# Kernel optimization log

Measured on AMD Instinct MI355X. Metric: run time of the kernel, lower is better.

The kernel has to match this reference:

```python
import jax, jax.numpy as jnp
import numpy as np

N = 8192
IN_DIM, HID_DIM, OUT_DIM = 32, 64, 16


def setup_inputs() -> dict:
    key = jax.random.key(0)
    k1, k2, k3, k4, k5, k6, k7 = jax.random.split(key, 7)
    s1 = 1.0 / np.sqrt(IN_DIM)
    s2 = 1.0 / np.sqrt(HID_DIM)
    return {
        "adj1": jax.random.normal(k1, (N, N), jnp.float32),
        "adj2": jax.random.normal(k2, (N, N), jnp.float32),
        "features": jax.random.normal(k3, (N, IN_DIM), jnp.float32),
        # gc1 linear (shared across both aggregation branches)
        "W1": jax.random.uniform(k4, (IN_DIM, HID_DIM), jnp.float32, -s1, s1),
        "b1": jax.random.uniform(k5, (HID_DIM,), jnp.float32, -s1, s1),
        # gc2 linear
        "W2": jax.random.uniform(k6, (HID_DIM, OUT_DIM), jnp.float32, -s2, s2),
        "b2": jax.random.uniform(k7, (OUT_DIM,), jnp.float32, -s2, s2),
    }


def _gc_layer(adj1, adj2, x, W, b):
    # branch 1: aggregate -> shared linear -> relu
    o1 = jax.nn.relu(jnp.matmul(adj1, x) @ W + b)
    # branch 2: same linear weights
    o2 = jax.nn.relu(jnp.matmul(adj2, x) @ W + b)
    return o1 + o2


def reference(adj1, adj2, features, W1, b1, W2, b2):
    h1 = _gc_layer(adj1, adj2, features, W1, b1)  # [N, HID_DIM]
    h2 = _gc_layer(adj1, adj2, h1, W2, b2)        # [N, OUT_DIM]
    return h2
```

## Files before the change

kernel.cpp:

```cpp
#include <hip/hip_runtime.h>
#include <stdint.h>

#define NN 8192
#define IN_DIM 32
#define HID_DIM 64
#define OUT_DIM 16

typedef __attribute__((ext_vector_type(8))) short short8;
typedef __attribute__((ext_vector_type(4))) float f32x4;

__device__ __forceinline__ short f2bf_bits(float x){
  uint32_t u = __builtin_bit_cast(uint32_t, x);
  u += 0x7FFFu + ((u >> 16) & 1u);
  return (short)(u >> 16);
}

__device__ __forceinline__ short8 cvt8(f32x4 lo, f32x4 hi){
  short8 r;
  r[0]=f2bf_bits(lo[0]); r[1]=f2bf_bits(lo[1]); r[2]=f2bf_bits(lo[2]); r[3]=f2bf_bits(lo[3]);
  r[4]=f2bf_bits(hi[0]); r[5]=f2bf_bits(hi[1]); r[6]=f2bf_bits(hi[2]); r[7]=f2bf_bits(hi[3]);
  return r;
}

__global__ __launch_bounds__(256) void k_g(const float* __restrict__ X, const float* __restrict__ W1,
                                           short* __restrict__ Gt){
  const int b    = blockIdx.x;
  const int rb   = (b & 127) * 64;
  const int cg   = b >> 7;
  const int lane = threadIdx.x & 63;
  const int c    = cg * 4 + (threadIdx.x >> 6);
  const int r    = rb + lane;
  const float* xr = X + (size_t)r * IN_DIM;
  float acc = 0.f;
  #pragma unroll
  for (int k = 0; k < IN_DIM; ++k)
    acc += xr[k] * W1[(size_t)k * HID_DIM + c];
  Gt[(size_t)c * NN + r] = f2bf_bits(acc);
}

template<int REV>
__global__ __launch_bounds__(64, 2) void mm64r(const float* __restrict__ adj1, const float* __restrict__ adj2,
                                               const short* __restrict__ Bt,
                                               float* __restrict__ P1, float* __restrict__ P2, int klen){
  __shared__ __align__(16) float sA[2][64 * 32];
  const int l     = threadIdx.x;
  const int strip = REV ? ((int)gridDim.x - 1 - (int)blockIdx.x) : (int)blockIdx.x;
  const int ks    = REV ? ((int)gridDim.y - 1 - (int)blockIdx.y) : (int)blockIdx.y;
  const int z     = REV ? (1 - (int)blockIdx.z) : (int)blockIdx.z;
  const float* __restrict__ adj = z ? adj2 : adj1;
  const int k0    = ks * klen;
  const int ngrp  = klen >> 5;
  const int phase = (strip + (z << 3)) & (ngrp - 1);
  const int rl    = l & 15;
  const int qh    = l >> 4;
  const int sr8   = l >> 3;
  const int sg    = (l & 7) ^ sr8;
  const size_t rowb = (size_t)strip * 64 * NN;

  auto gmap = [&](int t){
    const int tg = REV ? (phase + ngrp - 1 - t) : (phase + t);
    return tg & (ngrp - 1);
  };

  auto SL = [&](int t, f32x4 (&R)[8]){
    const int g = gmap(t);
    const float* base = adj + rowb + (size_t)(k0 + g * 32) + sg * 4;
    #pragma unroll
    for (int p = 0; p < 8; ++p)
      R[p] = *(const f32x4*)(base + (size_t)(p * 8 + sr8) * NN);
  };

  auto DW = [&](const f32x4 (&R)[8], float* buf){
    float* dst = buf + (l & 7) * 4;
    #pragma unroll
    for (int p = 0; p < 8; ++p)
      *(f32x4*)(dst + (p * 8 + sr8) * 32) = R[p];
  };

  auto BL = [&](int t, short8 (&d)[4]){
    const int g = gmap(t);
    const size_t bk = (size_t)(k0 + g * 32) + qh * 8;
    #pragma unroll
    for (int f = 0; f < 4; ++f)
      d[f] = *(const short8*)(Bt + (size_t)(f * 16 + rl) * NN + bk);
  };

  f32x4 acc[4][4];
  #pragma unroll
  for (int mi = 0; mi < 4; ++mi)
    #pragma unroll
    for (int f = 0; f < 4; ++f)
      acc[mi][f] = f32x4{0.f,0.f,0.f,0.f};

  auto compute = [&](const float* sa, const short8 (&b)[4]){
    #pragma unroll
    for (int mi = 0; mi < 4; ++mi){
      const int row = mi * 16 + rl;
      f32x4 lo = *(const f32x4*)(sa + row * 32 + (((qh * 2    ) ^ (rl & 7)) << 2));
      f32x4 hi = *(const f32x4*)(sa + row * 32 + (((qh * 2 + 1) ^ (rl & 7)) << 2));
      short8 fa = cvt8(lo, hi);
      #pragma unroll
      for (int f = 0; f < 4; ++f)
        acc[mi][f] = __builtin_amdgcn_mfma_f32_16x16x32_bf16(fa, b[f], acc[mi][f], 0, 0, 0);
    }
  };

  f32x4 SA[8];
  short8 bA[4], bB[4];

  SL(0, SA); BL(0, bA);

  #pragma unroll 1
  for (int t = 0; t < ngrp - 2; t += 2){
    asm volatile("s_waitcnt vmcnt(4)" ::: "memory");
    __builtin_amdgcn_sched_barrier(0);
    DW(SA, &sA[0][0]);
    SL(t + 1, SA);
    asm volatile("s_waitcnt vmcnt(8)" ::: "memory");
    __builtin_amdgcn_sched_barrier(0);
    BL(t + 1, bB);
    compute(&sA[0][0], bA);
    asm volatile("s_waitcnt vmcnt(4)" ::: "memory");
    __builtin_amdgcn_sched_barrier(0);
    DW(SA, &sA[1][0]);
    SL(t + 2, SA);
    asm volatile("s_waitcnt vmcnt(8)" ::: "memory");
    __builtin_amdgcn_sched_barrier(0);
    BL(t + 2, bA);
    compute(&sA[1][0], bB);
  }
  asm volatile("s_waitcnt vmcnt(4)" ::: "memory");
  __builtin_amdgcn_sched_barrier(0);
  DW(SA, &sA[0][0]);
  SL(ngrp - 1, SA);
  asm volatile("s_waitcnt vmcnt(8)" ::: "memory");
  __builtin_amdgcn_sched_barrier(0);
  BL(ngrp - 1, bB);
  compute(&sA[0][0], bA);
  asm volatile("s_waitcnt vmcnt(4)" ::: "memory");
  __builtin_amdgcn_sched_barrier(0);
  DW(SA, &sA[1][0]);
  asm volatile("s_waitcnt vmcnt(0)" ::: "memory");
  __builtin_amdgcn_sched_barrier(0);
  compute(&sA[1][0], bB);

  float* P = z ? P2 : P1;
  #pragma unroll
  for (int mi = 0; mi < 4; ++mi){
    const int orow = strip * 64 + mi * 16 + qh * 4;
    float* p = P + ((size_t)ks * NN + orow) * HID_DIM + rl;
    #pragma unroll
    for (int r = 0; r < 4; ++r){
      #pragma unroll
      for (int f = 0; f < 4; ++f)
        p[(size_t)r * HID_DIM + f * 16] = acc[mi][f][r];
    }
  }
}

__global__ __launch_bounds__(256) void l1_combine(const float* __restrict__ Y1p, const float* __restrict__ Y2p,
                                                  const float* __restrict__ b1,
                                                  short* __restrict__ H1t, int S){
  __shared__ float sH[64][65];
  const int tid = threadIdx.x, lane = tid & 63, wave = tid >> 6;
  const int rb = blockIdx.x * 64;
  const float bc = b1[lane];
  #pragma unroll 4
  for (int rq = 0; rq < 16; ++rq){
    const int r = rq * 4 + wave;
    const int row = rb + r;
    float s1 = 0.f, s2 = 0.f;
    for (int sp = 0; sp < S; ++sp){
      s1 += Y1p[((size_t)sp * NN + row) * HID_DIM + lane];
      s2 += Y2p[((size_t)sp * NN + row) * HID_DIM + lane];
    }
    sH[r][lane] = fmaxf(s1 + bc, 0.f) + fmaxf(s2 + bc, 0.f);
  }
  __syncthreads();
  #pragma unroll 4
  for (int i = 0; i < 16; ++i){
    const int c = wave * 16 + i;
    H1t[(size_t)c * NN + rb + lane] = f2bf_bits(sH[lane][c]);
  }
}

__global__ __launch_bounds__(256) void l2_combine(const float* __restrict__ Z1p, const float* __restrict__ Z2p,
                                                  const float* __restrict__ W2, const float* __restrict__ b2,
                                                  float* __restrict__ out, int S){
  __shared__ float sW[HID_DIM * OUT_DIM];
  __shared__ float sb[OUT_DIM];
  __shared__ float sz[4][2][HID_DIM];
  const int tid = threadIdx.x;
  for (int i = tid; i < HID_DIM * OUT_DIM; i += 256) sW[i] = W2[i];
  if (tid < OUT_DIM) sb[tid] = b2[tid];
  const int sub = tid >> 6, t = tid & 63;
  const int row = blockIdx.x * 4 + sub;
  float s1 = 0.f, s2 = 0.f;
  for (int sp = 0; sp < S; ++sp){
    s1 += Z1p[((size_t)sp * NN + row) * HID_DIM + t];
    s2 += Z2p[((size_t)sp * NN + row) * HID_DIM + t];
  }
  sz[sub][0][t] = s1;
  sz[sub][1][t] = s2;
  __syncthreads();
  if (t < OUT_DIM){
    float a = sb[t], b = sb[t];
    #pragma unroll
    for (int k = 0; k < HID_DIM; ++k){
      a += sz[sub][0][k] * sW[k * OUT_DIM + t];
      b += sz[sub][1][k] * sW[k * OUT_DIM + t];
    }
    out[(size_t)row * OUT_DIM + t] = fmaxf(a, 0.f) + fmaxf(b, 0.f);
  }
}

extern "C" void kernel_launch(void* const* d_in, const int* in_sizes, int n_in,
                              void* d_out, int out_size, void* d_ws, size_t ws_size,
                              hipStream_t stream){
  const float* adj1 = (const float*)d_in[0];
  const float* adj2 = (const float*)d_in[1];
  const float* X    = (const float*)d_in[2];
  const float* W1   = (const float*)d_in[3];
  const float* b1   = (const float*)d_in[4];
  const float* W2   = (const float*)d_in[5];
  const float* b2   = (const float*)d_in[6];
  float* out = (float*)d_out;

  char* ws = (char*)d_ws;
  short* Gt  = (short*)ws;
  short* H1t = (short*)(ws + (size_t)1024 * 1024);
  const size_t off = (size_t)2 * 1024 * 1024;

  int S = 8;
  while (S > 1 && off + (size_t)S * 4 * 1024 * 1024 > ws_size) S >>= 1;
  float* P1 = (float*)(ws + off);
  float* P2 = P1 + (size_t)S * NN * HID_DIM;
  const int klen = NN / S;

  k_g        <<<dim3(2048),          dim3(256), 0, stream>>>(X, W1, Gt);
  mm64r<0>   <<<dim3(NN / 64, S, 2), dim3(64),  0, stream>>>(adj1, adj2, Gt, P1, P2, klen);
  l1_combine <<<dim3(NN / 64),       dim3(256), 0, stream>>>(P1, P2, b1, H1t, S);
  mm64r<1>   <<<dim3(NN / 64, S, 2), dim3(64),  0, stream>>>(adj1, adj2, H1t, P1, P2, klen);
  l2_combine <<<dim3(NN / 4),        dim3(256), 0, stream>>>(P1, P2, W2, b2, out, S);
}
```

Before: 262.0 us.

## Repack adjacency to bf16 during first pass and reuse it in second pass

The first aggregation kernel now writes the bf16-converted adjacency tiles it already produces for the MFMAs out to workspace. A new second-pass kernel, mm2h, reads those half-width copies straight into LDS using global_load_lds, instead of re-reading the fp32 adjacency. It runs in reverse order, aiming to hit the recently written bf16 data in the last-level cache. This trades extra write traffic in pass one for halved read traffic in pass two, and needs a large workspace, with the old path kept as a fallback.

```diff
diff --git a/kernel.cpp b/kernel.cpp
--- a/kernel.cpp
+++ b/kernel.cpp
@@ -38,9 +38,10 @@
   Gt[(size_t)c * NN + r] = f2bf_bits(acc);
 }
 
-template<int REV>
+template<int REV, int REPACK>
 __global__ __launch_bounds__(64, 2) void mm64r(const float* __restrict__ adj1, const float* __restrict__ adj2,
                                                const short* __restrict__ Bt,
+                                               short* __restrict__ adjh1, short* __restrict__ adjh2,
                                                float* __restrict__ P1, float* __restrict__ P2, int klen){
   __shared__ __align__(16) float sA[2][64 * 32];
   const int l     = threadIdx.x;
@@ -48,6 +49,7 @@
   const int ks    = REV ? ((int)gridDim.y - 1 - (int)blockIdx.y) : (int)blockIdx.y;
   const int z     = REV ? (1 - (int)blockIdx.z) : (int)blockIdx.z;
   const float* __restrict__ adj = z ? adj2 : adj1;
+  short* __restrict__ adjh = z ? adjh2 : adjh1;
   const int k0    = ks * klen;
   const int ngrp  = klen >> 5;
   const int phase = (strip + (z << 3)) & (ngrp - 1);
@@ -92,13 +94,15 @@
     for (int f = 0; f < 4; ++f)
       acc[mi][f] = f32x4{0.f,0.f,0.f,0.f};
 
-  auto compute = [&](const float* sa, const short8 (&b)[4]){
+  auto compute = [&](int g, const float* sa, const short8 (&b)[4]){
     #pragma unroll
     for (int mi = 0; mi < 4; ++mi){
       const int row = mi * 16 + rl;
       f32x4 lo = *(const f32x4*)(sa + row * 32 + (((qh * 2    ) ^ (rl & 7)) << 2));
       f32x4 hi = *(const f32x4*)(sa + row * 32 + (((qh * 2 + 1) ^ (rl & 7)) << 2));
       short8 fa = cvt8(lo, hi);
+      if constexpr (REPACK)
+        *(short8*)(adjh + (size_t)(strip * 64 + mi * 16 + rl) * NN + (k0 + g * 32 + qh * 8)) = fa;
       #pragma unroll
       for (int f = 0; f < 4; ++f)
         acc[mi][f] = __builtin_amdgcn_mfma_f32_16x16x32_bf16(fa, b[f], acc[mi][f], 0, 0, 0);
@@ -109,40 +113,156 @@
   short8 bA[4], bB[4];
 
   SL(0, SA); BL(0, bA);
+  if constexpr (REPACK){
+    const int g0 = gmap(0);
+    const short8 zz = {0,0,0,0,0,0,0,0};
+    #pragma unroll
+    for (int mi = 0; mi < 4; ++mi)
+      *(short8*)(adjh + (size_t)(strip * 64 + mi * 16 + rl) * NN + (k0 + g0 * 32 + qh * 8)) = zz;
+  }
+
+  #define WAIT_A do{ if constexpr (REPACK) asm volatile("s_waitcnt vmcnt(8)" ::: "memory"); \
+                     else asm volatile("s_waitcnt vmcnt(4)" ::: "memory"); \
+                     __builtin_amdgcn_sched_barrier(0); }while(0)
+  #define WAIT_B do{ if constexpr (REPACK) asm volatile("s_waitcnt vmcnt(12)" ::: "memory"); \
+                     else asm volatile("s_waitcnt vmcnt(8)" ::: "memory"); \
+                     __builtin_amdgcn_sched_barrier(0); }while(0)
 
   #pragma unroll 1
   for (int t = 0; t < ngrp - 2; t += 2){
-    asm volatile("s_waitcnt vmcnt(4)" ::: "memory");
-    __builtin_amdgcn_sched_barrier(0);
+    WAIT_A;
     DW(SA, &sA[0][0]);
     SL(t + 1, SA);
-    asm volatile("s_waitcnt vmcnt(8)" ::: "memory");
-    __builtin_amdgcn_sched_barrier(0);
+    WAIT_B;
     BL(t + 1, bB);
-    compute(&sA[0][0], bA);
-    asm volatile("s_waitcnt vmcnt(4)" ::: "memory");
-    __builtin_amdgcn_sched_barrier(0);
+    compute(gmap(t), &sA[0][0], bA);
+    WAIT_A;
     DW(SA, &sA[1][0]);
     SL(t + 2, SA);
-    asm volatile("s_waitcnt vmcnt(8)" ::: "memory");
-    __builtin_amdgcn_sched_barrier(0);
+    WAIT_B;
     BL(t + 2, bA);
-    compute(&sA[1][0], bB);
-  }
-  asm volatile("s_waitcnt vmcnt(4)" ::: "memory");
-  __builtin_amdgcn_sched_barrier(0);
+    compute(gmap(t + 1), &sA[1][0], bB);
+  }
+  WAIT_A;
   DW(SA, &sA[0][0]);
   SL(ngrp - 1, SA);
-  asm volatile("s_waitcnt vmcnt(8)" ::: "memory");
+  WAIT_B;
+  BL(ngrp - 1, bB);
+  compute(gmap(ngrp - 2), &sA[0][0], bA);
+  WAIT_A;
+  DW(SA, &sA[1][0]);
+  if constexpr (REPACK) asm volatile("s_waitcnt vmcnt(4)" ::: "memory");
+  else                  asm volatile("s_waitcnt vmcnt(0)" ::: "memory");
   __builtin_amdgcn_sched_barrier(0);
-  BL(ngrp - 1, bB);
-  compute(&sA[0][0], bA);
-  asm volatile("s_waitcnt vmcnt(4)" ::: "memory");
+  compute(gmap(ngrp - 1), &sA[1][0], bB);
+  #undef WAIT_A
+  #undef WAIT_B
+
+  float* P = z ? P2 : P1;
+  #pragma unroll
+  for (int mi = 0; mi < 4; ++mi){
+    const int orow = strip * 64 + mi * 16 + qh * 4;
+    float* p = P + ((size_t)ks * NN + orow) * HID_DIM + rl;
+    #pragma unroll
+    for (int r = 0; r < 4; ++r){
+      #pragma unroll
+      for (int f = 0; f < 4; ++f)
+        p[(size_t)r * HID_DIM + f * 16] = acc[mi][f][r];
+    }
+  }
+}
+
+template<int REV>
+__global__ __launch_bounds__(64, 2) void mm2h(const short* __restrict__ A1, const short* __restrict__ A2,
+                                              const short* __restrict__ Bt,
+                                              float* __restrict__ P1, float* __restrict__ P2, int klen){
+  __shared__ __align__(16) short hA[2][64 * 64];
+  const int l     = threadIdx.x;
+  const int strip = REV ? ((int)gridDim.x - 1 - (int)blockIdx.x) : (int)blockIdx.x;
+  const int ks    = REV ? ((int)gridDim.y - 1 - (int)blockIdx.y) : (int)blockIdx.y;
+  const int z     = REV ? (1 - (int)blockIdx.z) : (int)blockIdx.z;
+  const short* __restrict__ A = z ? A2 : A1;
+  const int k0    = ks * klen;
+  const int ngrp  = klen >> 6;
+  const int phase = (strip + (z << 3)) & (ngrp - 1);
+  const int rl    = l & 15;
+  const int qh    = l >> 4;
+  const int sr    = l >> 3;
+  const int sgr   = (l & 7) ^ sr;
+  const size_t rowb = (size_t)strip * 64 * NN;
+
+  auto gmap = [&](int t){
+    const int tg = REV ? (phase + ngrp - 1 - t) : (phase + t);
+    return tg & (ngrp - 1);
+  };
+
+  auto SL = [&](int t, int buf){
+    const int g = gmap(t);
+    const size_t colb = (size_t)(k0 + g * 64);
+    #pragma unroll
+    for (int p = 0; p < 8; ++p){
+      const int row = p * 8 + sr;
+      const short* s = A + rowb + (size_t)row * NN + colb + sgr * 8;
+      __builtin_amdgcn_global_load_lds(
+          (const __attribute__((address_space(1))) void*)s,
+          (__attribute__((address_space(3))) void*)&hA[buf][p * 512 + l * 8], 16, 0, 0);
+    }
+  };
+
+  auto BL = [&](int t, short8 (&d)[2][4]){
+    const int g = gmap(t);
+    const size_t bk = (size_t)(k0 + g * 64) + qh * 8;
+    #pragma unroll
+    for (int j = 0; j < 2; ++j)
+      #pragma unroll
+      for (int f = 0; f < 4; ++f)
+        d[j][f] = *(const short8*)(Bt + (size_t)(f * 16 + rl) * NN + bk + j * 32);
+  };
+
+  f32x4 acc[4][4];
+  #pragma unroll
+  for (int mi = 0; mi < 4; ++mi)
+    #pragma unroll
+    for (int f = 0; f < 4; ++f)
+      acc[mi][f] = f32x4{0.f,0.f,0.f,0.f};
+
+  auto compute = [&](const short* sa, const short8 (&b)[2][4]){
+    #pragma unroll
+    for (int j = 0; j < 2; ++j){
+      #pragma unroll
+      for (int mi = 0; mi < 4; ++mi){
+        const int row = mi * 16 + rl;
+        const int c   = j * 4 + qh;
+        short8 fa = *(const short8*)(sa + row * 64 + ((c ^ (row & 7)) << 3));
+        #pragma unroll
+        for (int f = 0; f < 4; ++f)
+          acc[mi][f] = __builtin_amdgcn_mfma_f32_16x16x32_bf16(fa, b[j][f], acc[mi][f], 0, 0, 0);
+      }
+    }
+  };
+
+  short8 bA[2][4], bB[2][4];
+
+  BL(0, bA); SL(0, 0);
+
+  #pragma unroll 1
+  for (int t = 0; t < ngrp - 2; t += 2){
+    BL(t + 1, bB); SL(t + 1, 1);
+    asm volatile("s_waitcnt vmcnt(16)" ::: "memory");
+    __builtin_amdgcn_sched_barrier(0);
+    compute(&hA[0][0], bA);
+    BL(t + 2, bA); SL(t + 2, 0);
+    asm volatile("s_waitcnt vmcnt(16)" ::: "memory");
+    __builtin_amdgcn_sched_barrier(0);
+    compute(&hA[1][0], bB);
+  }
+  BL(ngrp - 1, bB); SL(ngrp - 1, 1);
+  asm volatile("s_waitcnt vmcnt(16)" ::: "memory");
   __builtin_amdgcn_sched_barrier(0);
-  DW(SA, &sA[1][0]);
+  compute(&hA[0][0], bA);
   asm volatile("s_waitcnt vmcnt(0)" ::: "memory");
   __builtin_amdgcn_sched_barrier(0);
-  compute(&sA[1][0], bB);
+  compute(&hA[1][0], bB);
 
   float* P = z ? P2 : P1;
   #pragma unroll
@@ -226,20 +346,35 @@
   const float* b2   = (const float*)d_in[6];
   float* out = (float*)d_out;
 
+  const size_t MB = 1024 * 1024;
   char* ws = (char*)d_ws;
   short* Gt  = (short*)ws;
-  short* H1t = (short*)(ws + (size_t)1024 * 1024);
-  const size_t off = (size_t)2 * 1024 * 1024;
-
-  int S = 8;
-  while (S > 1 && off + (size_t)S * 4 * 1024 * 1024 > ws_size) S >>= 1;
-  float* P1 = (float*)(ws + off);
-  float* P2 = P1 + (size_t)S * NN * HID_DIM;
-  const int klen = NN / S;
-
-  k_g        <<<dim3(2048),          dim3(256), 0, stream>>>(X, W1, Gt);
-  mm64r<0>   <<<dim3(NN / 64, S, 2), dim3(64),  0, stream>>>(adj1, adj2, Gt, P1, P2, klen);
-  l1_combine <<<dim3(NN / 64),       dim3(256), 0, stream>>>(P1, P2, b1, H1t, S);
-  mm64r<1>   <<<dim3(NN / 64, S, 2), dim3(64),  0, stream>>>(adj1, adj2, H1t, P1, P2, klen);
-  l2_combine <<<dim3(NN / 4),        dim3(256), 0, stream>>>(P1, P2, W2, b2, out, S);
-}
+  short* H1t = (short*)(ws + 1 * MB);
+
+  if (ws_size >= 291 * MB){
+    const int S = 8, klen = NN / 8;
+    float* P1 = (float*)(ws + 2 * MB);
+    float* P2 = P1 + (size_t)S * NN * HID_DIM;
+    short* adjh1 = (short*)(ws + 34 * MB);
+    short* adjh2 = (short*)(ws + 162 * MB);
+
+    k_g         <<<dim3(2048),          dim3(256), 0, stream>>>(X, W1, Gt);
+    mm64r<0, 1> <<<dim3(NN / 64, S, 2), dim3(64),  0, stream>>>(adj1, adj2, Gt, adjh1, adjh2, P1, P2, klen);
+    l1_combine  <<<dim3(NN / 64),       dim3(256), 0, stream>>>(P1, P2, b1, H1t, S);
+    mm2h<1>     <<<dim3(NN / 64, S, 2), dim3(64),  0, stream>>>(adjh1, adjh2, H1t, P1, P2, klen);
+    l2_combine  <<<dim3(NN / 4),        dim3(256), 0, stream>>>(P1, P2, W2, b2, out, S);
+  } else {
+    int S = 8;
+    const size_t off = 2 * MB;
+    while (S > 1 && off + (size_t)S * 4 * MB > ws_size) S >>= 1;
+    float* P1 = (float*)(ws + off);
+    float* P2 = P1 + (size_t)S * NN * HID_DIM;
+    const int klen = NN / S;
+
+    k_g         <<<dim3(2048),          dim3(256), 0, stream>>>(X, W1, Gt);
+    mm64r<0, 0> <<<dim3(NN / 64, S, 2), dim3(64),  0, stream>>>(adj1, adj2, Gt, nullptr, nullptr, P1, P2, klen);
+    l1_combine  <<<dim3(NN / 64),       dim3(256), 0, stream>>>(P1, P2, b1, H1t, S);
+    mm64r<1, 0> <<<dim3(NN / 64, S, 2), dim3(64),  0, stream>>>(adj1, adj2, H1t, nullptr, nullptr, P1, P2, klen);
+    l2_combine  <<<dim3(NN / 4),        dim3(256), 0, stream>>>(P1, P2, W2, b2, out, S);
+  }
+}
```

Result: slower. 355.6 us (+35.7%).
